# Kernel optimization log

Measured on AMD Instinct MI355X. Metric: run time of the kernel, lower is better.

Reference implementation:

```python
import jax, jax.numpy as jnp
import numpy as np

N = 20000      # n_nodes
L = 4          # lamb_len (number of decay rates)
M = 64         # memory_dimension (= message_dimension)
F = 128        # node feature dim
E = 128        # embedding_dimension
B = 100000     # number of interaction events in the batch
RAW = 2 * M * L + F + 1  # 641, raw message dim
H = RAW // 2   # MLP hidden dim


def setup_inputs() -> dict:
    key = jax.random.key(0)
    ks = jax.random.split(key, 18)
    s = lambda d: 1.0 / np.sqrt(d)
    inp = {
        "node_features": jax.random.normal(ks[0], (N, F), jnp.float32),
        "memory": jax.random.normal(ks[1], (N, L, M), jnp.float32) * 0.1,
        "last_update": jnp.zeros((N,), jnp.float32),
        "lambs": jnp.array([1.0, 0.1, 0.01, 0.001], jnp.float32),
        "theta": jnp.array([0.5], jnp.float32),
        "static_emb": jax.random.normal(ks[2], (N, E), jnp.float32),
        "W1": jax.random.normal(ks[3], (H, RAW), jnp.float32) * s(RAW),
        "b1": jnp.zeros((H,), jnp.float32),
        "W2": jax.random.normal(ks[4], (M, H), jnp.float32) * s(H),
        "b2": jnp.zeros((M,), jnp.float32),
        "We": jax.random.normal(ks[5], (M, L * M), jnp.float32) * s(L * M),
        "be": jnp.zeros((M,), jnp.float32),
        "Ws": jax.random.normal(ks[6], (E, M), jnp.float32) * s(M),
        "bs": jnp.zeros((E,), jnp.float32),
        "timestamps": jax.random.uniform(ks[7], (B,), jnp.float32) * 1000.0,
        "source_nodes": jax.random.randint(ks[8], (B,), 0, N),
        "target_nodes": jax.random.randint(ks[9], (B,), 0, N),
    }
    return inp


def reference(node_features, memory, last_update, lambs, theta, static_emb,
              W1, b1, W2, b2, We, be, Ws, bs,
              timestamps, source_nodes, target_nodes):
    n, l, m = memory.shape
    b = source_nodes.shape[0]
    mem_flat = memory.reshape(n, l * m)

    # ---- temporal memory gather + raw message build: [B, RAW] ----
    src_emb = mem_flat[source_nodes]
    tgt_emb = mem_flat[target_nodes]
    raw = jnp.concatenate(
        [src_emb, tgt_emb, node_features[target_nodes],
         jnp.ones((b, 1), memory.dtype)], axis=1)

    # ---- exp_lambs aggregation per source node ----
    t_node = jax.ops.segment_max(timestamps, source_nodes, num_segments=n)
    counts = jax.ops.segment_sum(jnp.ones_like(timestamps), source_nodes,
                                 num_segments=n)
    has = counts > 0
    t_node_safe = jnp.where(has, t_node, last_update)  # latest event time per node
    dt = t_node_safe[source_nodes] - timestamps        # [B], >= 0
    w = jnp.exp(-dt[:, None] * lambs[None, :])         # [B, L] decay weights
    # decayed sum of raw messages per node, per lambda: [N, L, RAW]
    agg = jnp.stack(
        [jax.ops.segment_sum(w[:, li:li + 1] * raw, source_nodes,
                             num_segments=n) for li in range(l)], axis=1)

    # ---- MLP message function: [N, L, M] ----
    h = jax.nn.relu(jnp.einsum('nlr,hr->nlh', agg, W1) + b1)
    msg = jnp.einsum('nlh,mh->nlm', h, W2) + b2

    # ---- exp memory update ----
    decay = jnp.exp(-(t_node_safe - last_update)[:, None] * lambs[None, :])  # [N, L]
    updated = memory * decay[..., None] + jnp.where(has[:, None, None], msg, 0.0)

    # ---- embedding fusion ----
    dyn = updated.reshape(n, l * m)
    e = jax.nn.leaky_relu(dyn @ We.T + be, negative_slope=0.01)
    s = jax.nn.leaky_relu(e @ Ws.T + bs, negative_slope=0.01)
    embeddings = theta * static_emb + (1.0 - theta) * s
    return embeddings
```

## Files before the change

### kernel.cpp

```cpp
#include <hip/hip_runtime.h>

constexpr int LDIM = 4;
constexpr int MDIM = 64;
constexpr int FDIM = 128;
constexpr int EDIM = 128;
constexpr int RAWD = 641;
constexpr int HDIM = 320;
constexpr int LM   = LDIM * MDIM;
constexpr int KXY  = LM + FDIM;
constexpr int NXY  = 2 * HDIM;

typedef _Float16 f16x8 __attribute__((ext_vector_type(8)));
typedef float    f32x4 __attribute__((ext_vector_type(4)));

constexpr float WSCALE  = 256.f;
constexpr float WSINV   = 1.f / 256.f;

__global__ void k_init(int* t_node_bits, int* counts, int* cursor2, int* cursor, int Nn)
{
    int n = blockIdx.x * blockDim.x + threadIdx.x;
    if (n < Nn) {
        t_node_bits[n] = 0xBF800000;
        counts[n]  = 0;
        cursor2[n] = 0;
    }
    if (n == 0) cursor[0] = 0;
}

__global__ void k_ev1(const int* __restrict__ src, const float* __restrict__ ts,
                      int* t_node_bits, int* counts, int Bev)
{
    int b = blockIdx.x * blockDim.x + threadIdx.x;
    if (b >= Bev) return;
    int s = src[b];
    atomicMax(&t_node_bits[s], __float_as_int(ts[b]));
    atomicAdd(&counts[s], 1);
}

__global__ void k_node(const int* __restrict__ t_node_bits, const int* __restrict__ counts,
                       const float* __restrict__ last_update, const float* __restrict__ lambs,
                       float* t_safe, float* decay, int* start, int* cursor, int Nn)
{
    int n = blockIdx.x * blockDim.x + threadIdx.x;
    if (n >= Nn) return;
    int c = counts[n];
    float lu = last_update[n];
    float tsn = (c > 0) ? __int_as_float(t_node_bits[n]) : lu;
    t_safe[n] = tsn;
    float d = tsn - lu;
    #pragma unroll
    for (int li = 0; li < LDIM; ++li)
        decay[n * LDIM + li] = expf(-d * lambs[li]);
    start[n] = atomicAdd(cursor, c);
}

__global__ void k_ev2(const int* __restrict__ src, const int* __restrict__ tgt,
                      const float* __restrict__ ts, const float* __restrict__ t_safe,
                      const int* __restrict__ start, int* cursor2,
                      const float* __restrict__ lambs,
                      int* sorted_tgt, float4* sorted_w, int Bev)
{
    int b = blockIdx.x * blockDim.x + threadIdx.x;
    if (b >= Bev) return;
    int s = src[b];
    int pos = start[s] + atomicAdd(&cursor2[s], 1);
    sorted_tgt[pos] = tgt[b];
    float dt = t_safe[s] - ts[b];
    sorted_w[pos] = make_float4(expf(-dt * lambs[0]), expf(-dt * lambs[1]),
                                expf(-dt * lambs[2]), expf(-dt * lambs[3]));
}

__global__ void k_half(const float* __restrict__ mem, const float* __restrict__ nf,
                       _Float16* __restrict__ A1, int total)
{
    int idx = blockIdx.x * blockDim.x + threadIdx.x;
    if (idx >= total) return;
    int n = idx / KXY, k = idx % KXY;
    float v = (k < LM) ? mem[(long)n * LM + k] : nf[(long)n * FDIM + (k - LM)];
    A1[idx] = (_Float16)v;
}

__global__ void k_prep(const float* __restrict__ W1, const float* __restrict__ W2,
                       const float* __restrict__ We, const float* __restrict__ Ws,
                       _Float16* WpH, _Float16* WpL, _Float16* W2H, _Float16* W2L,
                       _Float16* WeH, _Float16* WeL, _Float16* WsH, _Float16* WsL)
{
    int idx = blockIdx.x * blockDim.x + threadIdx.x;
    constexpr int T1 = NXY * KXY;
    constexpr int T2 = MDIM * HDIM;
    constexpr int T3 = MDIM * LM;
    constexpr int T4 = EDIM * MDIM;
    float v; _Float16 *H, *L; int o;
    if (idx < T1) {
        int n = idx / KXY, k = idx % KXY;
        if (n < HDIM) {
            v = (k < LM) ? W1[(long)n * RAWD + k] : 0.f;
        } else {
            int hh = n - HDIM;
            v = (k < LM) ? W1[(long)hh * RAWD + LM + k]
                         : W1[(long)hh * RAWD + 2 * LM + (k - LM)];
        }
        H = WpH; L = WpL; o = idx;
    } else if (idx < T1 + T2) {
        o = idx - T1; v = W2[o]; H = W2H; L = W2L;
    } else if (idx < T1 + T2 + T3) {
        o = idx - T1 - T2; v = We[o]; H = WeH; L = WeL;
    } else if (idx < T1 + T2 + T3 + T4) {
        o = idx - T1 - T2 - T3; v = Ws[o]; H = WsH; L = WsL;
    } else return;
    float xs = WSCALE * v;
    _Float16 hh = (_Float16)xs;
    _Float16 ll = (_Float16)(xs - (float)hh);
    H[o] = hh; L[o] = ll;
}

__global__ __launch_bounds__(256) void k_gather(
    const _Float16* __restrict__ C1, const float4* __restrict__ sorted_w,
    const int* __restrict__ sorted_tgt, const int* __restrict__ startb,
    const int* __restrict__ counts,
    const float* __restrict__ W1, const float* __restrict__ b1,
    _Float16* __restrict__ h, int Nn)
{
    const int lane = threadIdx.x & 63;
    const int wv   = threadIdx.x >> 6;
    float bb[5], wl[5];
    #pragma unroll
    for (int c = 0; c < 5; ++c) {
        int hi = c * 64 + lane;
        bb[c] = b1[hi];
        wl[c] = W1[(long)hi * RAWD + (RAWD - 1)];
    }
    for (int n = blockIdx.x * 4 + wv; n < Nn; n += gridDim.x * 4) {
        int cnt = counts[n];
        if (cnt == 0) continue;
        int st = startb[n];
        float z[5][4];
        float sw[4] = {0.f, 0.f, 0.f, 0.f};
        #pragma unroll
        for (int c = 0; c < 5; ++c)
            #pragma unroll
            for (int li = 0; li < 4; ++li) z[c][li] = 0.f;
        for (int e = 0; e < cnt; ++e) {
            float4 w = sorted_w[st + e];
            int    t = sorted_tgt[st + e];
            const _Float16* yr = C1 + (long)t * NXY + HDIM;
            sw[0] += w.x; sw[1] += w.y; sw[2] += w.z; sw[3] += w.w;
            #pragma unroll
            for (int c = 0; c < 5; ++c) {
                float yv = (float)yr[c * 64 + lane];
                z[c][0] += w.x * yv; z[c][1] += w.y * yv;
                z[c][2] += w.z * yv; z[c][3] += w.w * yv;
            }
        }
        #pragma unroll
        for (int c = 0; c < 5; ++c) {
            float xv = (float)C1[(long)n * NXY + c * 64 + lane] + wl[c];
            #pragma unroll
            for (int li = 0; li < 4; ++li) {
                float hv = xv * sw[li] + z[c][li] + bb[c];
                h[((long)n * LDIM + li) * HDIM + c * 64 + lane] = (_Float16)fmaxf(hv, 0.f);
            }
        }
    }
}

template <int BN, int EPI>
__global__ __launch_bounds__(256) void k_mgemm(
    const _Float16* __restrict__ Ag,
    const _Float16* __restrict__ Bgh, const _Float16* __restrict__ Bgl,
    _Float16* __restrict__ Ch, float* __restrict__ Cf,
    int M, int N, int K,
    const float* __restrict__ bias, const float* __restrict__ x1,
    const float* __restrict__ x2, const int* __restrict__ icnts,
    const float* __restrict__ theta)
{
    constexpr int BM = 128, BK = 32;
    constexpr int SN = BN / 32;
    __shared__ _Float16 Ash[BM * BK];
    __shared__ _Float16 Bsh[BN * BK], Bsl[BN * BK];
    const int tid  = threadIdx.x;
    const int w    = tid >> 6, lane = tid & 63;
    const int wm   = w >> 1,   wn   = w & 1;
    const int lrow = lane & 15, lq = lane >> 4;
    const long m0 = (long)blockIdx.x * BM;
    const int  n0 = blockIdx.y * BN;

    f32x4 acc[4][SN];
    #pragma unroll
    for (int s = 0; s < 4; ++s)
        #pragma unroll
        for (int t = 0; t < SN; ++t) acc[s][t] = (f32x4){0.f, 0.f, 0.f, 0.f};

    for (int k0 = 0; k0 < K; k0 += BK) {
        #pragma unroll
        for (int it = 0; it < 2; ++it) {
            int c = it * 256 + tid;
            int row = c >> 2, kc = c & 3;
            long gm = m0 + row; if (gm > M - 1) gm = M - 1;
            long goff = gm * (long)K + k0 + kc * 8;
            int soff = row * BK + ((kc ^ (row & 3)) << 3);
            *(int4*)&Ash[soff] = *(const int4*)(Ag + goff);
        }
        #pragma unroll
        for (int it = 0; it < BN / 64; ++it) {
            int c = it * 256 + tid;
            int row = c >> 2, kc = c & 3;
            long goff = (long)(n0 + row) * K + k0 + kc * 8;
            int soff = row * BK + ((kc ^ (row & 3)) << 3);
            *(int4*)&Bsh[soff] = *(const int4*)(Bgh + goff);
            *(int4*)&Bsl[soff] = *(const int4*)(Bgl + goff);
        }
        __syncthreads();

        f16x8 a[4], bh[SN], bl[SN];
        #pragma unroll
        for (int s = 0; s < 4; ++s) {
            int row = wm * 64 + s * 16 + lrow;
            int off = row * BK + ((lq ^ (row & 3)) << 3);
            a[s] = *(const f16x8*)&Ash[off];
        }
        #pragma unroll
        for (int t = 0; t < SN; ++t) {
            int row = wn * (BN / 2) + t * 16 + lrow;
            int off = row * BK + ((lq ^ (row & 3)) << 3);
            bh[t] = *(const f16x8*)&Bsh[off];
            bl[t] = *(const f16x8*)&Bsl[off];
        }
        #pragma unroll
        for (int s = 0; s < 4; ++s)
            #pragma unroll
            for (int t = 0; t < SN; ++t) {
                acc[s][t] = __builtin_amdgcn_mfma_f32_16x16x32_f16(a[s], bh[t], acc[s][t], 0, 0, 0);
                acc[s][t] = __builtin_amdgcn_mfma_f32_16x16x32_f16(a[s], bl[t], acc[s][t], 0, 0, 0);
            }
        __syncthreads();
    }

    float th = 0.f;
    if constexpr (EPI == 3) th = theta[0];
    #pragma unroll
    for (int s = 0; s < 4; ++s) {
        #pragma unroll
        for (int t = 0; t < SN; ++t) {
            #pragma unroll
            for (int r = 0; r < 4; ++r) {
                long grow = m0 + wm * 64 + s * 16 + lq * 4 + r;
                if (grow >= M) continue;
                int col = n0 + wn * (BN / 2) + t * 16 + lrow;
                float v = acc[s][t][r] * WSINV;
                long idx = grow * (long)N + col;
                if constexpr (EPI == 0) {
                    Ch[idx] = (_Float16)v;
                } else if constexpr (EPI == 1) {
                    float vb = v + bias[col];
                    bool has = icnts[grow >> 2] > 0;
                    float u = x1[idx] * x2[grow] + (has ? vb : 0.f);
                    Ch[idx] = (_Float16)u;
                } else if constexpr (EPI == 2) {
                    float u = v + bias[col];
                    u = u > 0.f ? u : 0.01f * u;
                    Ch[idx] = (_Float16)u;
                } else {
                    float u = v + bias[col];
                    u = u > 0.f ? u : 0.01f * u;
                    Cf[idx] = th * x1[idx] + (1.f - th) * u;
                }
            }
        }
    }
}

extern "C" void kernel_launch(void* const* d_in, const int* in_sizes, int n_in,
                              void* d_out, int out_size, void* d_ws, size_t ws_size,
                              hipStream_t stream)
{
    (void)n_in; (void)out_size; (void)ws_size;
    const float* node_features = (const float*)d_in[0];
    const float* memory        = (const float*)d_in[1];
    const float* last_update   = (const float*)d_in[2];
    const float* lambs         = (const float*)d_in[3];
    const float* theta         = (const float*)d_in[4];
    const float* static_emb    = (const float*)d_in[5];
    const float* W1            = (const float*)d_in[6];
    const float* b1            = (const float*)d_in[7];
    const float* W2            = (const float*)d_in[8];
    const float* b2            = (const float*)d_in[9];
    const float* We            = (const float*)d_in[10];
    const float* be            = (const float*)d_in[11];
    const float* Ws            = (const float*)d_in[12];
    const float* bs            = (const float*)d_in[13];
    const float* timestamps    = (const float*)d_in[14];
    const int*   src           = (const int*)d_in[15];
    const int*   tgt           = (const int*)d_in[16];
    float* out = (float*)d_out;

    const int Nn  = in_sizes[2];
    const int Bev = in_sizes[14];

    char* base = (char*)d_ws;
    size_t off = 0;
    auto take = [&](size_t bytes) -> void* {
        off = (off + 255) & ~(size_t)255;
        void* r = base + off;
        off += bytes;
        return r;
    };
    int*    t_node_bits = (int*)   take((size_t)Nn * 4);
    int*    counts      = (int*)   take((size_t)Nn * 4);
    int*    startb      = (int*)   take((size_t)Nn * 4);
    int*    cursor2     = (int*)   take((size_t)Nn * 4);
    int*    cursor      = (int*)   take(256);
    float*  t_safe      = (float*) take((size_t)Nn * 4);
    float*  decay       = (float*) take((size_t)Nn * LDIM * 4);
    int*    sorted_tgt  = (int*)   take((size_t)Bev * 4);
    float4* sorted_w    = (float4*)take((size_t)Bev * 16);
    _Float16* WpH = (_Float16*)take((size_t)NXY * KXY * 2);
    _Float16* WpL = (_Float16*)take((size_t)NXY * KXY * 2);
    _Float16* W2H = (_Float16*)take((size_t)MDIM * HDIM * 2);
    _Float16* W2L = (_Float16*)take((size_t)MDIM * HDIM * 2);
    _Float16* WeH = (_Float16*)take((size_t)MDIM * LM * 2);
    _Float16* WeL = (_Float16*)take((size_t)MDIM * LM * 2);
    _Float16* WsH = (_Float16*)take((size_t)EDIM * MDIM * 2);
    _Float16* WsL = (_Float16*)take((size_t)EDIM * MDIM * 2);
    _Float16* A1  = (_Float16*)take((size_t)Nn * KXY * 2);
    _Float16* C1  = (_Float16*)take((size_t)Nn * NXY * 2);
    _Float16* hbuf= (_Float16*)take((size_t)Nn * LDIM * HDIM * 2);
    _Float16* updh= (_Float16*)take((size_t)Nn * LM * 2);
    _Float16* ebuf= (_Float16*)take((size_t)Nn * MDIM * 2);

    const int tb = 256;
    k_init<<<(Nn + tb - 1) / tb, tb, 0, stream>>>(t_node_bits, counts, cursor2, cursor, Nn);
    k_ev1<<<(Bev + tb - 1) / tb, tb, 0, stream>>>(src, timestamps, t_node_bits, counts, Bev);
    k_node<<<(Nn + tb - 1) / tb, tb, 0, stream>>>(t_node_bits, counts, last_update, lambs,
                                                  t_safe, decay, startb, cursor, Nn);
    k_ev2<<<(Bev + tb - 1) / tb, tb, 0, stream>>>(src, tgt, timestamps, t_safe,
                                                  startb, cursor2, lambs,
                                                  sorted_tgt, sorted_w, Bev);
    const int preptot = NXY * KXY + MDIM * HDIM + MDIM * LM + EDIM * MDIM;
    k_prep<<<(preptot + tb - 1) / tb, tb, 0, stream>>>(W1, W2, We, Ws,
                                                       WpH, WpL, W2H, W2L,
                                                       WeH, WeL, WsH, WsL);
    const int packtot = Nn * KXY;
    k_half<<<(packtot + tb - 1) / tb, tb, 0, stream>>>(memory, node_features, A1, packtot);

    const int mb1 = (Nn + 127) / 128;

    k_mgemm<128, 0><<<dim3(mb1, NXY / 128), 256, 0, stream>>>(
        A1, WpH, WpL, C1, nullptr, Nn, NXY, KXY,
        nullptr, nullptr, nullptr, nullptr, nullptr);

    k_gather<<<5000, 256, 0, stream>>>(C1, sorted_w, sorted_tgt, startb, counts,
                                       W1, b1, hbuf, Nn);

    k_mgemm<64, 1><<<dim3(Nn * LDIM / 128, 1), 256, 0, stream>>>(
        hbuf, W2H, W2L, updh, nullptr, Nn * LDIM, MDIM, HDIM,
        b2, memory, decay, counts, nullptr);

    k_mgemm<64, 2><<<dim3(mb1, 1), 256, 0, stream>>>(
        updh, WeH, WeL, ebuf, nullptr, Nn, MDIM, LM,
        be, nullptr, nullptr, nullptr, nullptr);

    k_mgemm<128, 3><<<dim3(mb1, 1), 256, 0, stream>>>(
        ebuf, WsH, WsL, nullptr, out, Nn, EDIM, MDIM,
        bs, static_emb, nullptr, nullptr, theta);
}
```

Baseline: 299.4 us.

## Retune GEMM tiles, vectorize gather, fuse fp16 packing into weight prep

The GEMM kernel is generalized to configurable block and warp tiles, with 64-row blocks for more blocks on the small-N GEMMs, and the LDS swizzle now keys on row>>1. The gather kernel loads and stores four fp16 values per lane at once instead of strided scalars. The memory/feature fp16 packing is merged into the weight-prep launch, saving one kernel launch. The memory-update epilogue reads memory from the fp16 packed copy instead of the fp32 input, which cuts traffic but adds fp16 rounding error on the memory term.

```diff
diff --git a/kernel.cpp b/kernel.cpp
--- a/kernel.cpp
+++ b/kernel.cpp
@@ -11,6 +11,7 @@
 constexpr int NXY  = 2 * HDIM;
 
 typedef _Float16 f16x8 __attribute__((ext_vector_type(8)));
+typedef _Float16 f16x4 __attribute__((ext_vector_type(4)));
 typedef float    f32x4 __attribute__((ext_vector_type(4)));
 
 constexpr float WSCALE  = 256.f;
@@ -70,48 +71,50 @@
                                 expf(-dt * lambs[2]), expf(-dt * lambs[3]));
 }
 
-__global__ void k_half(const float* __restrict__ mem, const float* __restrict__ nf,
-                       _Float16* __restrict__ A1, int total)
-{
-    int idx = blockIdx.x * blockDim.x + threadIdx.x;
-    if (idx >= total) return;
-    int n = idx / KXY, k = idx % KXY;
-    float v = (k < LM) ? mem[(long)n * LM + k] : nf[(long)n * FDIM + (k - LM)];
-    A1[idx] = (_Float16)v;
-}
-
 __global__ void k_prep(const float* __restrict__ W1, const float* __restrict__ W2,
                        const float* __restrict__ We, const float* __restrict__ Ws,
+                       const float* __restrict__ mem, const float* __restrict__ nf,
                        _Float16* WpH, _Float16* WpL, _Float16* W2H, _Float16* W2L,
-                       _Float16* WeH, _Float16* WeL, _Float16* WsH, _Float16* WsL)
+                       _Float16* WeH, _Float16* WeL, _Float16* WsH, _Float16* WsL,
+                       _Float16* A1, int packtot)
 {
     int idx = blockIdx.x * blockDim.x + threadIdx.x;
     constexpr int T1 = NXY * KXY;
     constexpr int T2 = MDIM * HDIM;
     constexpr int T3 = MDIM * LM;
     constexpr int T4 = EDIM * MDIM;
-    float v; _Float16 *H, *L; int o;
-    if (idx < T1) {
-        int n = idx / KXY, k = idx % KXY;
-        if (n < HDIM) {
-            v = (k < LM) ? W1[(long)n * RAWD + k] : 0.f;
+    constexpr int TW = T1 + T2 + T3 + T4;
+    if (idx < TW) {
+        float v; _Float16 *H, *L; int o;
+        if (idx < T1) {
+            int n = idx / KXY, k = idx % KXY;
+            if (n < HDIM) {
+                v = (k < LM) ? W1[(long)n * RAWD + k] : 0.f;
+            } else {
+                int hh = n - HDIM;
+                v = (k < LM) ? W1[(long)hh * RAWD + LM + k]
+                             : W1[(long)hh * RAWD + 2 * LM + (k - LM)];
+            }
+            H = WpH; L = WpL; o = idx;
+        } else if (idx < T1 + T2) {
+            o = idx - T1; v = W2[o]; H = W2H; L = W2L;
+        } else if (idx < T1 + T2 + T3) {
+            o = idx - T1 - T2; v = We[o]; H = WeH; L = WeL;
         } else {
-            int hh = n - HDIM;
-            v = (k < LM) ? W1[(long)hh * RAWD + LM + k]
-                         : W1[(long)hh * RAWD + 2 * LM + (k - LM)];
-        }
-        H = WpH; L = WpL; o = idx;
-    } else if (idx < T1 + T2) {
-        o = idx - T1; v = W2[o]; H = W2H; L = W2L;
-    } else if (idx < T1 + T2 + T3) {
-        o = idx - T1 - T2; v = We[o]; H = WeH; L = WeL;
-    } else if (idx < T1 + T2 + T3 + T4) {
-        o = idx - T1 - T2 - T3; v = Ws[o]; H = WsH; L = WsL;
-    } else return;
-    float xs = WSCALE * v;
-    _Float16 hh = (_Float16)xs;
-    _Float16 ll = (_Float16)(xs - (float)hh);
-    H[o] = hh; L[o] = ll;
+            o = idx - T1 - T2 - T3; v = Ws[o]; H = WsH; L = WsL;
+        }
+        float xs = WSCALE * v;
+        _Float16 hh = (_Float16)xs;
+        _Float16 ll = (_Float16)(xs - (float)hh);
+        H[o] = hh; L[o] = ll;
+    } else {
+        int r = idx - TW;
+        if (r < packtot) {
+            int n = r / KXY, k = r % KXY;
+            float v = (k < LM) ? mem[(long)n * LM + k] : nf[(long)n * FDIM + (k - LM)];
+            A1[r] = (_Float16)v;
+        }
+    }
 }
 
 __global__ __launch_bounds__(256) void k_gather(
@@ -123,111 +126,129 @@
 {
     const int lane = threadIdx.x & 63;
     const int wv   = threadIdx.x >> 6;
-    float bb[5], wl[5];
+    float4 b4 = *(const float4*)&b1[lane * 4];
+    float bbA[4] = {b4.x, b4.y, b4.z, b4.w};
+    float bbB = b1[256 + lane];
+    float wlA[4], wlB;
     #pragma unroll
-    for (int c = 0; c < 5; ++c) {
-        int hi = c * 64 + lane;
-        bb[c] = b1[hi];
-        wl[c] = W1[(long)hi * RAWD + (RAWD - 1)];
-    }
+    for (int j = 0; j < 4; ++j)
+        wlA[j] = W1[(long)(lane * 4 + j) * RAWD + (RAWD - 1)];
+    wlB = W1[(long)(256 + lane) * RAWD + (RAWD - 1)];
+
     for (int n = blockIdx.x * 4 + wv; n < Nn; n += gridDim.x * 4) {
         int cnt = counts[n];
         if (cnt == 0) continue;
         int st = startb[n];
-        float z[5][4];
-        float sw[4] = {0.f, 0.f, 0.f, 0.f};
-        #pragma unroll
-        for (int c = 0; c < 5; ++c)
-            #pragma unroll
-            for (int li = 0; li < 4; ++li) z[c][li] = 0.f;
+        float zA[4][4], zB[4], sw[4];
+        #pragma unroll
+        for (int li = 0; li < 4; ++li) { zB[li] = 0.f; sw[li] = 0.f; }
+        #pragma unroll
+        for (int j = 0; j < 4; ++j)
+            #pragma unroll
+            for (int li = 0; li < 4; ++li) zA[j][li] = 0.f;
+
         for (int e = 0; e < cnt; ++e) {
             float4 w = sorted_w[st + e];
             int    t = sorted_tgt[st + e];
             const _Float16* yr = C1 + (long)t * NXY + HDIM;
+            f16x4 yA = *(const f16x4*)(yr + lane * 4);
+            float  yB = (float)yr[256 + lane];
+            float wf[4] = {w.x, w.y, w.z, w.w};
             sw[0] += w.x; sw[1] += w.y; sw[2] += w.z; sw[3] += w.w;
             #pragma unroll
-            for (int c = 0; c < 5; ++c) {
-                float yv = (float)yr[c * 64 + lane];
-                z[c][0] += w.x * yv; z[c][1] += w.y * yv;
-                z[c][2] += w.z * yv; z[c][3] += w.w * yv;
+            for (int j = 0; j < 4; ++j) {
+                float yv = (float)yA[j];
+                #pragma unroll
+                for (int li = 0; li < 4; ++li) zA[j][li] += wf[li] * yv;
             }
-        }
-        #pragma unroll
-        for (int c = 0; c < 5; ++c) {
-            float xv = (float)C1[(long)n * NXY + c * 64 + lane] + wl[c];
-            #pragma unroll
-            for (int li = 0; li < 4; ++li) {
-                float hv = xv * sw[li] + z[c][li] + bb[c];
-                h[((long)n * LDIM + li) * HDIM + c * 64 + lane] = (_Float16)fmaxf(hv, 0.f);
-            }
-        }
-    }
-}
-
-template <int BN, int EPI>
+            #pragma unroll
+            for (int li = 0; li < 4; ++li) zB[li] += wf[li] * yB;
+        }
+
+        const _Float16* xr = C1 + (long)n * NXY;
+        f16x4 xA4 = *(const f16x4*)(xr + lane * 4);
+        float xB = (float)xr[256 + lane] + wlB;
+        float xA[4];
+        #pragma unroll
+        for (int j = 0; j < 4; ++j) xA[j] = (float)xA4[j] + wlA[j];
+        #pragma unroll
+        for (int li = 0; li < 4; ++li) {
+            _Float16* hr = h + ((long)n * LDIM + li) * HDIM;
+            f16x4 hv;
+            #pragma unroll
+            for (int j = 0; j < 4; ++j)
+                hv[j] = (_Float16)fmaxf(xA[j] * sw[li] + zA[j][li] + bbA[j], 0.f);
+            *(f16x4*)(hr + lane * 4) = hv;
+            hr[256 + lane] = (_Float16)fmaxf(xB * sw[li] + zB[li] + bbB, 0.f);
+        }
+    }
+}
+
+template <int BM, int BN, int WM, int WN, int EPI>
 __global__ __launch_bounds__(256) void k_mgemm(
     const _Float16* __restrict__ Ag,
     const _Float16* __restrict__ Bgh, const _Float16* __restrict__ Bgl,
     _Float16* __restrict__ Ch, float* __restrict__ Cf,
     int M, int N, int K,
-    const float* __restrict__ bias, const float* __restrict__ x1,
-    const float* __restrict__ x2, const int* __restrict__ icnts,
-    const float* __restrict__ theta)
-{
-    constexpr int BM = 128, BK = 32;
-    constexpr int SN = BN / 32;
+    const float* __restrict__ bias, const _Float16* __restrict__ x1h,
+    const float* __restrict__ x1f, const float* __restrict__ x2,
+    const int* __restrict__ icnts, const float* __restrict__ theta)
+{
+    constexpr int BK = 32;
+    constexpr int WROWS = BM / WM, WCOLS = BN / WN;
+    constexpr int SM = WROWS / 16, SN = WCOLS / 16;
+    static_assert(WM * WN == 4 && SM * 16 == WROWS && SN * 16 == WCOLS, "");
+    static_assert((BM * 4) % 256 == 0 && (BN * 4) % 256 == 0, "");
     __shared__ _Float16 Ash[BM * BK];
     __shared__ _Float16 Bsh[BN * BK], Bsl[BN * BK];
     const int tid  = threadIdx.x;
     const int w    = tid >> 6, lane = tid & 63;
-    const int wm   = w >> 1,   wn   = w & 1;
+    const int wm   = w / WN,   wn   = w % WN;
     const int lrow = lane & 15, lq = lane >> 4;
     const long m0 = (long)blockIdx.x * BM;
     const int  n0 = blockIdx.y * BN;
 
-    f32x4 acc[4][SN];
+    f32x4 acc[SM][SN];
     #pragma unroll
-    for (int s = 0; s < 4; ++s)
+    for (int s = 0; s < SM; ++s)
         #pragma unroll
         for (int t = 0; t < SN; ++t) acc[s][t] = (f32x4){0.f, 0.f, 0.f, 0.f};
 
     for (int k0 = 0; k0 < K; k0 += BK) {
         #pragma unroll
-        for (int it = 0; it < 2; ++it) {
-            int c = it * 256 + tid;
+        for (int f0 = 0; f0 < BM * 4; f0 += 256) {
+            int c = f0 + tid;
             int row = c >> 2, kc = c & 3;
             long gm = m0 + row; if (gm > M - 1) gm = M - 1;
-            long goff = gm * (long)K + k0 + kc * 8;
-            int soff = row * BK + ((kc ^ (row & 3)) << 3);
-            *(int4*)&Ash[soff] = *(const int4*)(Ag + goff);
-        }
-        #pragma unroll
-        for (int it = 0; it < BN / 64; ++it) {
-            int c = it * 256 + tid;
+            int soff = row * BK + ((kc ^ ((row >> 1) & 3)) << 3);
+            *(int4*)&Ash[soff] = *(const int4*)(Ag + gm * (long)K + k0 + kc * 8);
+        }
+        #pragma unroll
+        for (int f0 = 0; f0 < BN * 4; f0 += 256) {
+            int c = f0 + tid;
             int row = c >> 2, kc = c & 3;
             long goff = (long)(n0 + row) * K + k0 + kc * 8;
-            int soff = row * BK + ((kc ^ (row & 3)) << 3);
+            int soff = row * BK + ((kc ^ ((row >> 1) & 3)) << 3);
             *(int4*)&Bsh[soff] = *(const int4*)(Bgh + goff);
             *(int4*)&Bsl[soff] = *(const int4*)(Bgl + goff);
         }
         __syncthreads();
 
-        f16x8 a[4], bh[SN], bl[SN];
-        #pragma unroll
-        for (int s = 0; s < 4; ++s) {
-            int row = wm * 64 + s * 16 + lrow;
-            int off = row * BK + ((lq ^ (row & 3)) << 3);
-            a[s] = *(const f16x8*)&Ash[off];
+        f16x8 a[SM], bh[SN], bl[SN];
+        #pragma unroll
+        for (int s = 0; s < SM; ++s) {
+            int row = wm * WROWS + s * 16 + lrow;
+            a[s] = *(const f16x8*)&Ash[row * BK + ((lq ^ ((row >> 1) & 3)) << 3)];
         }
         #pragma unroll
         for (int t = 0; t < SN; ++t) {
-            int row = wn * (BN / 2) + t * 16 + lrow;
-            int off = row * BK + ((lq ^ (row & 3)) << 3);
+            int row = wn * WCOLS + t * 16 + lrow;
+            int off = row * BK + ((lq ^ ((row >> 1) & 3)) << 3);
             bh[t] = *(const f16x8*)&Bsh[off];
             bl[t] = *(const f16x8*)&Bsl[off];
         }
         #pragma unroll
-        for (int s = 0; s < 4; ++s)
+        for (int s = 0; s < SM; ++s)
             #pragma unroll
             for (int t = 0; t < SN; ++t) {
                 acc[s][t] = __builtin_amdgcn_mfma_f32_16x16x32_f16(a[s], bh[t], acc[s][t], 0, 0, 0);
@@ -239,14 +260,14 @@
     float th = 0.f;
     if constexpr (EPI == 3) th = theta[0];
     #pragma unroll
-    for (int s = 0; s < 4; ++s) {
+    for (int s = 0; s < SM; ++s) {
         #pragma unroll
         for (int t = 0; t < SN; ++t) {
             #pragma unroll
             for (int r = 0; r < 4; ++r) {
-                long grow = m0 + wm * 64 + s * 16 + lq * 4 + r;
+                long grow = m0 + wm * WROWS + s * 16 + lq * 4 + r;
                 if (grow >= M) continue;
-                int col = n0 + wn * (BN / 2) + t * 16 + lrow;
+                int col = n0 + wn * WCOLS + t * 16 + lrow;
                 float v = acc[s][t][r] * WSINV;
                 long idx = grow * (long)N + col;
                 if constexpr (EPI == 0) {
@@ -254,7 +275,8 @@
                 } else if constexpr (EPI == 1) {
                     float vb = v + bias[col];
                     bool has = icnts[grow >> 2] > 0;
-                    float u = x1[idx] * x2[grow] + (has ? vb : 0.f);
+                    float mv = (float)x1h[(grow >> 2) * KXY + (grow & 3) * MDIM + col];
+                    float u = mv * x2[grow] + (has ? vb : 0.f);
                     Ch[idx] = (_Float16)u;
                 } else if constexpr (EPI == 2) {
                     float u = v + bias[col];
@@ -263,7 +285,7 @@
                 } else {
                     float u = v + bias[col];
                     u = u > 0.f ? u : 0.01f * u;
-                    Cf[idx] = th * x1[idx] + (1.f - th) * u;
+                    Cf[idx] = th * x1f[idx] + (1.f - th) * u;
                 }
             }
         }
@@ -336,31 +358,32 @@
     k_ev2<<<(Bev + tb - 1) / tb, tb, 0, stream>>>(src, tgt, timestamps, t_safe,
                                                   startb, cursor2, lambs,
                                                   sorted_tgt, sorted_w, Bev);
-    const int preptot = NXY * KXY + MDIM * HDIM + MDIM * LM + EDIM * MDIM;
+    const int packtot = Nn * KXY;
+    const int preptot = NXY * KXY + MDIM * HDIM + MDIM * LM + EDIM * MDIM + packtot;
     k_prep<<<(preptot + tb - 1) / tb, tb, 0, stream>>>(W1, W2, We, Ws,
+                                                       memory, node_features,
                                                        WpH, WpL, W2H, W2L,
-                                                       WeH, WeL, WsH, WsL);
-    const int packtot = Nn * KXY;
-    k_half<<<(packtot + tb - 1) / tb, tb, 0, stream>>>(memory, node_features, A1, packtot);
-
-    const int mb1 = (Nn + 127) / 128;
-
-    k_mgemm<128, 0><<<dim3(mb1, NXY / 128), 256, 0, stream>>>(
+                                                       WeH, WeL, WsH, WsL,
+                                                       A1, packtot);
+
+    const int mb64 = (Nn + 63) / 64;
+
+    k_mgemm<64, 128, 1, 4, 0><<<dim3(mb64, NXY / 128), 256, 0, stream>>>(
         A1, WpH, WpL, C1, nullptr, Nn, NXY, KXY,
-        nullptr, nullptr, nullptr, nullptr, nullptr);
+        nullptr, nullptr, nullptr, nullptr, nullptr, nullptr);
 
     k_gather<<<5000, 256, 0, stream>>>(C1, sorted_w, sorted_tgt, startb, counts,
                                        W1, b1, hbuf, Nn);
 
-    k_mgemm<64, 1><<<dim3(Nn * LDIM / 128, 1), 256, 0, stream>>>(
+    k_mgemm<64, 64, 2, 2, 1><<<dim3(Nn * LDIM / 64, 1), 256, 0, stream>>>(
         hbuf, W2H, W2L, updh, nullptr, Nn * LDIM, MDIM, HDIM,
-        b2, memory, decay, counts, nullptr);
-
-    k_mgemm<64, 2><<<dim3(mb1, 1), 256, 0, stream>>>(
+        b2, A1, nullptr, decay, counts, nullptr);
+
+    k_mgemm<64, 64, 2, 2, 2><<<dim3(mb64, 1), 256, 0, stream>>>(
         updh, WeH, WeL, ebuf, nullptr, Nn, MDIM, LM,
-        be, nullptr, nullptr, nullptr, nullptr);
-
-    k_mgemm<128, 3><<<dim3(mb1, 1), 256, 0, stream>>>(
+        be, nullptr, nullptr, nullptr, nullptr, nullptr);
+
+    k_mgemm<64, 128, 1, 4, 3><<<dim3(mb64, 1), 256, 0, stream>>>(
         ebuf, WsH, WsL, nullptr, out, Nn, EDIM, MDIM,
-        bs, static_emb, nullptr, nullptr, theta);
-}
+        bs, nullptr, static_emb, nullptr, nullptr, theta);
+}
```

After: 276.2 us. 7.8% less time.
